# Optimization experiments

Measured on AMD Instinct MI355X. Metric: run time of the kernel, lower is better.

## Reference

```python
import jax, jax.numpy as jnp
import numpy as np

L, BS, D, NH = 1024, 4, 1024, 16
DH = D // NH
H = max(DH, L)  # big=True in DenseSynthesizer -> h = max(head_dim, n_tokens)


def setup_inputs() -> dict:
    key = jax.random.key(0)
    ks = jax.random.split(key, 10)
    s = 0.02
    x = jax.random.normal(ks[0], (L, BS, D), dtype=jnp.float32)
    # additive causal mask (n_tokens, n_tokens)
    causal = jnp.tril(jnp.ones((L, L), dtype=bool))
    attention_mask = jnp.where(causal, 0.0, -1e9).astype(jnp.float32)
    Wi = jax.random.normal(ks[1], (2 * D, D), dtype=jnp.float32) * s
    bi = jnp.zeros((2 * D,), dtype=jnp.float32)
    w1 = jax.random.normal(ks[2], (NH, DH, H), dtype=jnp.float32) * s
    b1 = jnp.zeros((NH, H), dtype=jnp.float32)
    w2 = jax.random.normal(ks[3], (NH, H, L), dtype=jnp.float32) * s
    b2 = jnp.zeros((NH, L), dtype=jnp.float32)
    Wo = jax.random.normal(ks[4], (D, D), dtype=jnp.float32) * s
    bo = jnp.zeros((D,), dtype=jnp.float32)
    return {"x": x, "attention_mask": attention_mask, "Wi": Wi, "bi": bi,
            "w1": w1, "b1": b1, "w2": w2, "b2": b2, "Wo": Wo, "bo": bo}


def reference(x, attention_mask, Wi, bi, w1, b1, w2, b2, Wo, bo):
    l, bs, d = x.shape
    nh, dh, h = w1.shape
    # input projection, chunk into synthesizer input q and values v
    proj = x @ Wi.T + bi                                    # (l, bs, 2d)
    q, v = jnp.split(proj, 2, axis=-1)
    q = q.reshape(l, bs, nh, dh).transpose(1, 0, 2, 3)      # (bs, l, nh, dh)
    v = v.reshape(l, bs * nh, dh).transpose(1, 0, 2)        # (bs*nh, l, dh), n = b*nh + k
    # DenseSynthesizer: per-head two-layer MLP producing attention logits
    hid = jax.nn.relu(jnp.einsum('blkd,kdh->blkh', q, w1) + b1)
    logits = jnp.einsum('blkh,khm->blkm', hid, w2) + b2     # (bs, l, nh, n_tokens)
    logits = logits[..., :l]
    # faithful to torch transpose(0,3).view(l,l,bs*nh).transpose(0,2):
    # flattened batch-head index is m = k*bs + b (head-major)
    logits = logits.transpose(2, 0, 1, 3).reshape(bs * nh, l, l)
    logits = logits + attention_mask[None, :, :]
    probs = jax.nn.softmax(logits, axis=-1)                 # dropout p=0 (eval)
    out = jnp.matmul(probs, v)                              # (bs*nh, l, dh)
    out = out.transpose(1, 0, 2).reshape(l, bs, d)
    return out @ Wo.T + bo
```

## Files before the change

kernel.cpp:

```cpp
#include <hip/hip_runtime.h>

typedef unsigned short u16;
typedef short bf16x8 __attribute__((ext_vector_type(8)));
typedef float f32x4 __attribute__((ext_vector_type(4)));

#define BSZ 4
#define DD 1024
#define LLL 1024

__device__ __forceinline__ float bf2f(u16 u) {
    union { unsigned int i; float f; } w;
    w.i = ((unsigned int)u) << 16;
    return w.f;
}
__device__ __forceinline__ u16 f2bf(float f) {
    union { float fl; unsigned int i; } w;
    w.fl = f;
    w.i += 0x7fffu + ((w.i >> 16) & 1u);
    return (u16)(w.i >> 16);
}

__device__ __forceinline__ void load_lds16(const u16* g, u16* l) {
    __builtin_amdgcn_global_load_lds(
        (const __attribute__((address_space(1))) unsigned int*)g,
        (__attribute__((address_space(3))) unsigned int*)l, 16, 0, 0);
}

__global__ void cvt_all(const float* __restrict__ x, const float* __restrict__ Wi,
                        const float* __restrict__ Wo, u16* __restrict__ xb,
                        u16* __restrict__ wib, u16* __restrict__ wob) {
    int b = blockIdx.x;
    const float* in; u16* out;
    if (b < 4096)      { in = x;  out = xb; }
    else if (b < 6144) { in = Wi; out = wib; b -= 4096; }
    else               { in = Wo; out = wob; b -= 6144; }
    const size_t i = ((size_t)b * 256 + threadIdx.x) * 4;
    const float4 v = *(const float4*)(in + i);
    ushort4 o;
    o.x = f2bf(v.x); o.y = f2bf(v.y); o.z = f2bf(v.z); o.w = f2bf(v.w);
    *(ushort4*)(out + i) = o;
}

__global__ void transpose_cvt(const float* __restrict__ in, u16* __restrict__ out,
                              int R, int C) {
    __shared__ float tile[32][33];
    const size_t base = (size_t)blockIdx.z * R * C;
    const int c0 = blockIdx.x << 5, r0 = blockIdx.y << 5;
    const int tx = threadIdx.x & 31, ty = threadIdx.x >> 5;
    #pragma unroll
    for (int i = 0; i < 32; i += 8)
        tile[ty + i][tx] = in[base + (size_t)(r0 + ty + i) * C + c0 + tx];
    __syncthreads();
    #pragma unroll
    for (int i = 0; i < 32; i += 8)
        out[base + (size_t)(c0 + ty + i) * R + r0 + tx] = f2bf(tile[tx][ty + i]);
}

__global__ void build_vt(const u16* __restrict__ proj, u16* __restrict__ vt) {
    __shared__ u16 tile[64][66];
    const int t = threadIdx.x;
    const int m0 = blockIdx.x << 6;
    const int jj = blockIdx.y;
    const int b = jj >> 4, k = jj & 15;
    const int tx = t & 63, ty = t >> 6;
    #pragma unroll
    for (int mi = ty; mi < 64; mi += 4)
        tile[mi][tx] = proj[(size_t)((m0 + mi) * BSZ + b) * 2048 + 1024 + k * 64 + tx];
    __syncthreads();
    #pragma unroll
    for (int di = ty; di < 64; di += 4)
        vt[((size_t)jj * 80 + di) * 1024 + m0 + tx] = tile[tx][di];
    #pragma unroll
    for (int di = 64 + ty; di < 80; di += 4)
        vt[((size_t)jj * 80 + di) * 1024 + m0 + tx] = (di == 64) ? 0x3F80 : 0;
}

template<int OUT_F32, int RELU>
__global__ __launch_bounds__(256, 2) void gemm_bf16_nt(
    const u16* __restrict__ A, int lda, long long sA,
    const u16* __restrict__ B, int ldb, long long sB,
    const float* __restrict__ bias, int sBias,
    void* __restrict__ C, int ldc, long long sC,
    int K)
{
    __shared__ u16 As[128 * 64];
    __shared__ u16 Bs[128 * 64];
    const int t = threadIdx.x;
    const int z = blockIdx.z;
    const u16* Ab = A + (size_t)z * sA + (size_t)blockIdx.x * 128 * lda;
    const u16* Bb = B + (size_t)z * sB + (size_t)blockIdx.y * 128 * ldb;
    const int wave = t >> 6, lane = t & 63;
    const int wrow = (wave >> 1) << 6;
    const int wcol = (wave & 1) << 6;
    const int lr = lane & 15, lq = lane >> 4;
    const int srow = t >> 3;
    const int gchunk = (t & 7) ^ (srow & 7);
    const u16* ApG = Ab + (size_t)srow * lda + gchunk * 8;
    const u16* BpG = Bb + (size_t)srow * ldb + gchunk * 8;
    u16* AsD = &As[t * 8];
    u16* BsD = &Bs[t * 8];
    const int o0 = ((lq    ) ^ (lr & 7)) * 8;
    const int o1 = ((lq + 4) ^ (lr & 7)) * 8;

    f32x4 acc[4][4];
    #pragma unroll
    for (int i = 0; i < 4; i++)
        #pragma unroll
        for (int j = 0; j < 4; j++)
            acc[i][j] = (f32x4){0.f, 0.f, 0.f, 0.f};

    for (int k0 = 0; k0 < K; k0 += 64) {
        __syncthreads();
        #pragma unroll
        for (int j = 0; j < 4; j++) {
            load_lds16(ApG + (size_t)j * 32 * lda + k0, AsD + j * 2048);
            load_lds16(BpG + (size_t)j * 32 * ldb + k0, BsD + j * 2048);
        }
        __syncthreads();
        #pragma unroll
        for (int s = 0; s < 2; s++) {
            const int oo = s ? o1 : o0;
            bf16x8 af[4], bfv[4];
            #pragma unroll
            for (int i = 0; i < 4; i++)
                af[i] = *(const bf16x8*)&As[(wrow + i * 16 + lr) * 64 + oo];
            #pragma unroll
            for (int j = 0; j < 4; j++)
                bfv[j] = *(const bf16x8*)&Bs[(wcol + j * 16 + lr) * 64 + oo];
            #pragma unroll
            for (int i = 0; i < 4; i++)
                #pragma unroll
                for (int j = 0; j < 4; j++)
                    acc[i][j] = __builtin_amdgcn_mfma_f32_16x16x32_bf16(
                        af[i], bfv[j], acc[i][j], 0, 0, 0);
        }
    }

    const float* biasb = bias + (size_t)z * sBias;
    const size_t row0 = (size_t)blockIdx.x * 128 + wrow + lq * 4;
    const int col0 = blockIdx.y * 128 + wcol + lr;
    #pragma unroll
    for (int j = 0; j < 4; j++) {
        const int col = col0 + j * 16;
        const float bb = biasb[col];
        #pragma unroll
        for (int i = 0; i < 4; i++) {
            #pragma unroll
            for (int r = 0; r < 4; r++) {
                const size_t row = row0 + i * 16 + r;
                float v = acc[i][j][r] + bb;
                if (RELU) v = fmaxf(v, 0.f);
                const size_t idx = row * (size_t)ldc + col;
                if (OUT_F32) ((float*)C)[(size_t)z * sC + idx] = v;
                else         ((u16*)C)[(size_t)z * sC + idx] = f2bf(v);
            }
        }
    }
}

__global__ __launch_bounds__(256, 2) void fused_attn(
    const u16* __restrict__ proj,
    const u16* __restrict__ w1t,
    const float* __restrict__ b1,
    const u16* __restrict__ w2t,
    const float* __restrict__ b2,
    const u16* __restrict__ vt,
    u16* __restrict__ attn)
{
    __shared__ u16 As2[64 * 64];
    __shared__ u16 W1s[64 * 64];
    __shared__ u16 BsPs[256 * 64];
    const int t = threadIdx.x;
    const int kq = blockIdx.x;
    const int pair = blockIdx.y;
    const int wave = t >> 6, lane = t & 63;
    const int lr = lane & 15, lq = lane >> 4;
    const int srow = t >> 3;
    const int gch = (t & 7) ^ (srow & 7);
    const int o0 = ((lq    ) ^ (lr & 7)) * 8;
    const int o1 = ((lq + 4) ^ (lr & 7)) * 8;
    const int bv = kq >> 2;
    const int kvb = 4 * (kq & 3);
    const int hrow = (wave & 1) * 32;
    const int hcol = (wave >> 1) * 32;
    const u16* wb  = w2t + (size_t)kq * 1048576 + (size_t)srow * 1024 + gch * 8;
    const u16* w1b = w1t + (size_t)kq * 65536   + (size_t)srow * 64   + gch * 8;
    const float* b1b = b1 + kq * 1024;
    const float* b2b = b2 + kq * 1024;

    for (int part = 0; part < 2; part++) {
        const int s = part ? (63 - pair) : pair;
        const int l0 = s << 4;
        const int nt = (s >> 4) + 1;
        bf16x8 qf[2][2];
        #pragma unroll
        for (int i = 0; i < 2; i++) {
            const u16* qsrc = proj
                + ((size_t)((l0 + lr) * 4 + 2 * (wave & 1) + i)) * 2048
                + kq * 64 + lq * 8;
            qf[i][0] = *(const bf16x8*)qsrc;
            qf[i][1] = *(const bf16x8*)(qsrc + 32);
        }
        f32x4 o[5];
        #pragma unroll
        for (int j = 0; j < 5; j++) o[j] = (f32x4){0.f, 0.f, 0.f, 0.f};

        for (int mt = 0; mt < nt; mt++) {
            f32x4 acc[4][4];
            #pragma unroll
            for (int i = 0; i < 4; i++)
                #pragma unroll
                for (int j = 0; j < 4; j++)
                    acc[i][j] = (f32x4){0.f, 0.f, 0.f, 0.f};
            for (int k0 = 0; k0 < 1024; k0 += 64) {
                __syncthreads();
                float b1v[2];
                #pragma unroll
                for (int j2 = 0; j2 < 2; j2++)
                    b1v[j2] = b1b[k0 + hcol + j2 * 16 + lr];
                load_lds16(w1b + (size_t)k0 * 64,        &W1s[t * 8]);
                load_lds16(w1b + (size_t)k0 * 64 + 2048, &W1s[2048 + t * 8]);
                #pragma unroll
                for (int j2 = 0; j2 < 8; j2++)
                    load_lds16(wb + (size_t)(mt * 256 + j2 * 32) * 1024 + k0,
                               &BsPs[j2 * 2048 + t * 8]);
                asm volatile("s_waitcnt vmcnt(8)" ::: "memory");
                __builtin_amdgcn_s_barrier();
                __builtin_amdgcn_sched_barrier(0);
                {
                    f32x4 ah[2][2];
                    #pragma unroll
                    for (int i = 0; i < 2; i++)
                        #pragma unroll
                        for (int j2 = 0; j2 < 2; j2++)
                            ah[i][j2] = (f32x4){0.f, 0.f, 0.f, 0.f};
                    #pragma unroll
                    for (int kk = 0; kk < 2; kk++) {
                        const int oo = kk ? o1 : o0;
                        #pragma unroll
                        for (int j2 = 0; j2 < 2; j2++) {
                            const bf16x8 bw = *(const bf16x8*)
                                &W1s[(hcol + j2 * 16 + lr) * 64 + oo];
                            #pragma unroll
                            for (int i = 0; i < 2; i++)
                                ah[i][j2] = __builtin_amdgcn_mfma_f32_16x16x32_bf16(
                                    qf[i][kk], bw, ah[i][j2], 0, 0, 0);
                        }
                    }
                    #pragma unroll
                    for (int i = 0; i < 2; i++) {
                        const int rtb = hrow + i * 16 + lq * 4;
                        #pragma unroll
                        for (int j2 = 0; j2 < 2; j2++) {
                            const int ch = (hcol >> 3) + j2 * 2 + (lr >> 3);
                            #pragma unroll
                            for (int rg = 0; rg < 4; rg++) {
                                const float v = fmaxf(ah[i][j2][rg] + b1v[j2], 0.f);
                                const int row = rtb + rg;
                                As2[row * 64 + ((ch ^ (row & 7)) << 3) +
                                    (lr & 7)] = f2bf(v);
                            }
                        }
                    }
                }
                asm volatile("s_waitcnt vmcnt(0) lgkmcnt(0)" ::: "memory");
                __builtin_amdgcn_s_barrier();
                __builtin_amdgcn_sched_barrier(0);
                #pragma unroll
                for (int s2 = 0; s2 < 2; s2++) {
                    const int oo = s2 ? o1 : o0;
                    bf16x8 af[4], bfv[4];
                    #pragma unroll
                    for (int i = 0; i < 4; i++)
                        af[i] = *(const bf16x8*)
                            &As2[(i * 16 + lr) * 64 + oo];
                    #pragma unroll
                    for (int j = 0; j < 4; j++)
                        bfv[j] = *(const bf16x8*)
                            &BsPs[(wave * 64 + j * 16 + lr) * 64 + oo];
                    #pragma unroll
                    for (int i = 0; i < 4; i++)
                        #pragma unroll
                        for (int j = 0; j < 4; j++)
                            acc[i][j] = __builtin_amdgcn_mfma_f32_16x16x32_bf16(
                                af[i], bfv[j], acc[i][j], 0, 0, 0);
                }
            }
            __syncthreads();
            float b2v[4];
            #pragma unroll
            for (int j = 0; j < 4; j++)
                b2v[j] = b2b[mt * 256 + wave * 64 + j * 16 + lr];
            #pragma unroll
            for (int i = 0; i < 4; i++) {
                #pragma unroll
                for (int j = 0; j < 4; j++) {
                    const int cp = wave * 64 + j * 16 + lr;
                    const int m = mt * 256 + cp;
                    const int cb = cp & 7;
                    const int cc = cp >> 3;
                    #pragma unroll
                    for (int rr = 0; rr < 4; rr++) {
                        const int rt = i * 16 + lq * 4 + rr;
                        const int l = l0 + lq * 4 + rr;
                        const float e = __expf(acc[i][j][rr] + b2v[j]);
                        BsPs[rt * 256 + cb + ((cc ^ (rt & 7)) << 3)]
                            = (m <= l) ? f2bf(e) : (u16)0;
                    }
                }
            }
            __syncthreads();
            {
                const u16* vbb = vt + (size_t)(kq * 4 + wave) * 80 * 1024
                               + (size_t)mt * 256 + lq * 8;
                const int rt = wave * 16 + lr;
                #pragma unroll
                for (int kc = 0; kc < 8; kc++) {
                    const bf16x8 a = *(const bf16x8*)
                        &BsPs[rt * 256 + ((((kc << 2) + lq) ^ (rt & 7)) << 3)];
                    #pragma unroll
                    for (int j = 0; j < 5; j++) {
                        const bf16x8 b = *(const bf16x8*)
                            (vbb + (size_t)(j * 16 + lr) * 1024 + kc * 32);
                        o[j] = __builtin_amdgcn_mfma_f32_16x16x32_bf16(
                            a, b, o[j], 0, 0, 0);
                    }
                }
            }
        }
        {
            const int bq = wave;
            float sden[4];
            #pragma unroll
            for (int rr = 0; rr < 4; rr++)
                sden[rr] = __shfl(o[4][rr], lq << 4);
            #pragma unroll
            for (int j = 0; j < 4; j++) {
                #pragma unroll
                for (int rr = 0; rr < 4; rr++) {
                    const int l = l0 + lq * 4 + rr;
                    attn[(size_t)(l * BSZ + bv) * 1024 + (kvb + bq) * 64 + j * 16 + lr]
                        = f2bf(o[j][rr] / sden[rr]);
                }
            }
        }
    }
}

extern "C" void kernel_launch(void* const* d_in, const int* in_sizes, int n_in,
                              void* d_out, int out_size, void* d_ws, size_t ws_size,
                              hipStream_t stream)
{
    (void)in_sizes; (void)n_in; (void)out_size; (void)ws_size;
    const float* x  = (const float*)d_in[0];
    const float* Wi = (const float*)d_in[2];
    const float* bi = (const float*)d_in[3];
    const float* w1 = (const float*)d_in[4];
    const float* b1 = (const float*)d_in[5];
    const float* w2 = (const float*)d_in[6];
    const float* b2 = (const float*)d_in[7];
    const float* Wo = (const float*)d_in[8];
    const float* bo = (const float*)d_in[9];

    u16* x_b    = (u16*)d_ws;
    u16* Wi_b   = x_b    + (size_t)4194304;
    u16* w1t    = Wi_b   + (size_t)2097152;
    u16* w2t    = w1t    + (size_t)1048576;
    u16* Wo_b   = w2t    + (size_t)16777216;
    u16* proj_b = Wo_b   + (size_t)1048576;
    u16* attn_b = proj_b + (size_t)8388608;
    u16* vt     = attn_b + (size_t)4194304;

    cvt_all<<<7168, 256, 0, stream>>>(x, Wi, Wo, x_b, Wi_b, Wo_b);
    transpose_cvt<<<dim3(32,  2, 16), 256, 0, stream>>>(w1, w1t, 64,   1024);
    transpose_cvt<<<dim3(32, 32, 16), 256, 0, stream>>>(w2, w2t, 1024, 1024);

    gemm_bf16_nt<0, 0><<<dim3(32, 16, 1), 256, 0, stream>>>(
        x_b, 1024, 0, Wi_b, 1024, 0, bi, 0, (void*)proj_b, 2048, 0, 1024);

    build_vt<<<dim3(16, 64), 256, 0, stream>>>(proj_b, vt);

    fused_attn<<<dim3(16, 32), 256, 0, stream>>>(
        proj_b, w1t, b1, w2t, b2, vt, attn_b);

    gemm_bf16_nt<1, 0><<<dim3(32, 8, 1), 256, 0, stream>>>(
        attn_b, 1024, 0, Wo_b, 1024, 0, bo, 0, d_out, 1024, 0, 1024);
}
```

Measured before the change: 379.4 us.

## Double-buffer w2 tiles in LDS with next-step prefetch

Splits the shared w2/probability buffer into two LDS buffers and prefetches the next k-step's w2 tile, or the first tile of the next m-tile, while the current step computes. The vmcnt(0) wait before the second GEMM becomes an lgkmcnt-only wait, so global loads overlap the hidden-layer MFMA and the logits MFMA. The probability tile is now aliased onto the second buffer. LDS use grows to about 80KB per block, which may limit occupancy at two blocks per CU.

Measured after the change: 430.7 us. +13.5%, slower.

```diff
diff --git a/kernel.cpp b/kernel.cpp
--- a/kernel.cpp
+++ b/kernel.cpp
@@ -169,7 +169,8 @@
 {
     __shared__ u16 As2[64 * 64];
     __shared__ u16 W1s[64 * 64];
-    __shared__ u16 BsPs[256 * 64];
+    __shared__ u16 Bs[2 * 16384];
+    u16* Ps = &Bs[16384];
     const int t = threadIdx.x;
     const int kq = blockIdx.x;
     const int pair = blockIdx.y;
@@ -188,6 +189,13 @@
     const float* b1b = b1 + kq * 1024;
     const float* b2b = b2 + kq * 1024;
 
+    auto STAGE_BS = [&](int bbuf, int mtt, int k0) {
+        #pragma unroll
+        for (int j2 = 0; j2 < 8; j2++)
+            load_lds16(wb + (size_t)(mtt * 256 + j2 * 32) * 1024 + k0,
+                       &Bs[bbuf * 16384 + j2 * 2048 + t * 8]);
+    };
+
     for (int part = 0; part < 2; part++) {
         const int s = part ? (63 - pair) : pair;
         const int l0 = s << 4;
@@ -212,28 +220,31 @@
                 #pragma unroll
                 for (int j = 0; j < 4; j++)
                     acc[i][j] = (f32x4){0.f, 0.f, 0.f, 0.f};
-            for (int k0 = 0; k0 < 1024; k0 += 64) {
+            for (int i = 0; i < 16; i++) {
+                const int k0 = i * 64;
                 __syncthreads();
+                if (i == 0 && mt == 0)
+                    STAGE_BS(0, 0, 0);
                 float b1v[2];
                 #pragma unroll
                 for (int j2 = 0; j2 < 2; j2++)
                     b1v[j2] = b1b[k0 + hcol + j2 * 16 + lr];
                 load_lds16(w1b + (size_t)k0 * 64,        &W1s[t * 8]);
                 load_lds16(w1b + (size_t)k0 * 64 + 2048, &W1s[2048 + t * 8]);
-                #pragma unroll
-                for (int j2 = 0; j2 < 8; j2++)
-                    load_lds16(wb + (size_t)(mt * 256 + j2 * 32) * 1024 + k0,
-                               &BsPs[j2 * 2048 + t * 8]);
-                asm volatile("s_waitcnt vmcnt(8)" ::: "memory");
+                const int has_next = (i < 15) | (mt + 1 < nt);
+                if (i < 15)            STAGE_BS((i + 1) & 1, mt, k0 + 64);
+                else if (mt + 1 < nt)  STAGE_BS(0, mt + 1, 0);
+                if (has_next) asm volatile("s_waitcnt vmcnt(8)" ::: "memory");
+                else          asm volatile("s_waitcnt vmcnt(0)" ::: "memory");
                 __builtin_amdgcn_s_barrier();
                 __builtin_amdgcn_sched_barrier(0);
                 {
                     f32x4 ah[2][2];
                     #pragma unroll
-                    for (int i = 0; i < 2; i++)
+                    for (int i2 = 0; i2 < 2; i2++)
                         #pragma unroll
                         for (int j2 = 0; j2 < 2; j2++)
-                            ah[i][j2] = (f32x4){0.f, 0.f, 0.f, 0.f};
+                            ah[i2][j2] = (f32x4){0.f, 0.f, 0.f, 0.f};
                     #pragma unroll
                     for (int kk = 0; kk < 2; kk++) {
                         const int oo = kk ? o1 : o0;
@@ -242,20 +253,20 @@
                             const bf16x8 bw = *(const bf16x8*)
                                 &W1s[(hcol + j2 * 16 + lr) * 64 + oo];
                             #pragma unroll
-                            for (int i = 0; i < 2; i++)
-                                ah[i][j2] = __builtin_amdgcn_mfma_f32_16x16x32_bf16(
-                                    qf[i][kk], bw, ah[i][j2], 0, 0, 0);
+                            for (int i2 = 0; i2 < 2; i2++)
+                                ah[i2][j2] = __builtin_amdgcn_mfma_f32_16x16x32_bf16(
+                                    qf[i2][kk], bw, ah[i2][j2], 0, 0, 0);
                         }
                     }
                     #pragma unroll
-                    for (int i = 0; i < 2; i++) {
-                        const int rtb = hrow + i * 16 + lq * 4;
+                    for (int i2 = 0; i2 < 2; i2++) {
+                        const int rtb = hrow + i2 * 16 + lq * 4;
                         #pragma unroll
                         for (int j2 = 0; j2 < 2; j2++) {
                             const int ch = (hcol >> 3) + j2 * 2 + (lr >> 3);
                             #pragma unroll
                             for (int rg = 0; rg < 4; rg++) {
-                                const float v = fmaxf(ah[i][j2][rg] + b1v[j2], 0.f);
+                                const float v = fmaxf(ah[i2][j2][rg] + b1v[j2], 0.f);
                                 const int row = rtb + rg;
                                 As2[row * 64 + ((ch ^ (row & 7)) << 3) +
                                     (lr & 7)] = f2bf(v);
@@ -263,27 +274,28 @@
                         }
                     }
                 }
-                asm volatile("s_waitcnt vmcnt(0) lgkmcnt(0)" ::: "memory");
+                asm volatile("s_waitcnt lgkmcnt(0)" ::: "memory");
                 __builtin_amdgcn_s_barrier();
                 __builtin_amdgcn_sched_barrier(0);
+                const u16* Bsb = &Bs[(i & 1) * 16384];
                 #pragma unroll
                 for (int s2 = 0; s2 < 2; s2++) {
                     const int oo = s2 ? o1 : o0;
                     bf16x8 af[4], bfv[4];
                     #pragma unroll
-                    for (int i = 0; i < 4; i++)
-                        af[i] = *(const bf16x8*)
-                            &As2[(i * 16 + lr) * 64 + oo];
+                    for (int i2 = 0; i2 < 4; i2++)
+                        af[i2] = *(const bf16x8*)
+                            &As2[(i2 * 16 + lr) * 64 + oo];
                     #pragma unroll
                     for (int j = 0; j < 4; j++)
                         bfv[j] = *(const bf16x8*)
-                            &BsPs[(wave * 64 + j * 16 + lr) * 64 + oo];
-                    #pragma unroll
-                    for (int i = 0; i < 4; i++)
+                            &Bsb[(wave * 64 + j * 16 + lr) * 64 + oo];
+                    #pragma unroll
+                    for (int i2 = 0; i2 < 4; i2++)
                         #pragma unroll
                         for (int j = 0; j < 4; j++)
-                            acc[i][j] = __builtin_amdgcn_mfma_f32_16x16x32_bf16(
-                                af[i], bfv[j], acc[i][j], 0, 0, 0);
+                            acc[i2][j] = __builtin_amdgcn_mfma_f32_16x16x32_bf16(
+                                af[i2], bfv[j], acc[i2][j], 0, 0, 0);
                 }
             }
             __syncthreads();
@@ -304,7 +316,7 @@
                         const int rt = i * 16 + lq * 4 + rr;
                         const int l = l0 + lq * 4 + rr;
                         const float e = __expf(acc[i][j][rr] + b2v[j]);
-                        BsPs[rt * 256 + cb + ((cc ^ (rt & 7)) << 3)]
+                        Ps[rt * 256 + cb + ((cc ^ (rt & 7)) << 3)]
                             = (m <= l) ? f2bf(e) : (u16)0;
                     }
                 }
@@ -317,7 +329,7 @@
                 #pragma unroll
                 for (int kc = 0; kc < 8; kc++) {
                     const bf16x8 a = *(const bf16x8*)
-                        &BsPs[rt * 256 + ((((kc << 2) + lq) ^ (rt & 7)) << 3)];
+                        &Ps[rt * 256 + ((((kc << 2) + lq) ^ (rt & 7)) << 3)];
                     #pragma unroll
                     for (int j = 0; j < 5; j++) {
                         const bf16x8 b = *(const bf16x8*)
```
